# Kernel optimization log

Hardware: AMD Instinct MI355X
Metric: run time of the kernel (lower is better)

Reference implementation:

```python
import jax, jax.numpy as jnp
import numpy as np

N = 50000      # nodes
E = 800000     # edges
C = 128        # dim_feat / channels
D = 256        # dim_dense
OUT = 2        # dim_out
L = 5          # num_layers - 1 GCN2Conv layers
ALPHA = 0.1    # main_param -> GCN2Conv alpha; theta=None -> beta=1.0
SLOPE = 0.01   # LeakyReLU default negative slope


def setup_inputs() -> dict:
    key = jax.random.key(0)
    ks = jax.random.split(key, 6)
    x = jax.random.normal(ks[0], (N, C), jnp.float32)
    edge_index = jax.random.randint(ks[1], (2, E), 0, N, jnp.int32)
    conv_weights = jax.random.normal(ks[2], (L, C, C), jnp.float32) * (1.0 / np.sqrt(C))
    w_dense = jax.random.normal(ks[3], (C, D), jnp.float32) * (1.0 / np.sqrt(C))
    b_dense = jnp.zeros((D,), jnp.float32)
    w_out = jax.random.normal(ks[4], (D, OUT), jnp.float32) * (1.0 / np.sqrt(D))
    b_out = jnp.zeros((OUT,), jnp.float32)
    return dict(x=x, edge_index=edge_index, conv_weights=conv_weights,
                w_dense=w_dense, b_dense=b_dense, w_out=w_out, b_out=b_out)


def _gcn_norm(edge_index, num_nodes):
    """Symmetric gcn_norm with self-loops: returns row, col, D^-1/2 * D^-1/2 edge weights."""
    loop = jnp.arange(num_nodes, dtype=edge_index.dtype)
    row = jnp.concatenate([edge_index[0], loop])  # sources
    col = jnp.concatenate([edge_index[1], loop])  # targets (aggregation index)
    ones = jnp.ones(row.shape[0], jnp.float32)
    deg = jax.ops.segment_sum(ones, col, num_segments=num_nodes)
    dinv = jnp.where(deg > 0, jax.lax.rsqrt(jnp.maximum(deg, 1e-12)), 0.0)
    return row, col, dinv[row] * dinv[col]


def reference(x, edge_index, conv_weights, w_dense, b_dense, w_out, b_out):
    num_nodes = x.shape[0]
    row, col, norm = _gcn_norm(edge_index, num_nodes)
    x0 = x
    for l in range(conv_weights.shape[0]):
        # propagate: h[i] = sum_{j->i} norm * x[j]   (gather -> scatter-add)
        h = jax.ops.segment_sum(norm[:, None] * x[row], col, num_segments=num_nodes)
        # GCN2Conv with shared_weights=True, beta=1 (theta=None): out = ((1-a)h + a*x0) @ W
        out = (1.0 - ALPHA) * h + ALPHA * x0
        x = jax.nn.leaky_relu(out @ conv_weights[l], negative_slope=SLOPE)
    x = x @ w_dense + b_dense
    return x @ w_out + b_out
```

## Files before the change

kernel.cpp:

```cpp
#include <hip/hip_runtime.h>
#include <hip/hip_fp16.h>

#define C 128
#define NOUT 2
#define ALPHA 0.1f
#define SLOPE 0.01f
#define ZP 136

typedef _Float16 half4v __attribute__((ext_vector_type(4)));
typedef float float4v __attribute__((ext_vector_type(4)));


__global__ __launch_bounds__(256) void count_prep_kernel(
    const int* __restrict__ col, int* __restrict__ cnt, int* __restrict__ rank, int E,
    const float* __restrict__ x, __half* __restrict__ xh, int n,
    const float* __restrict__ W, _Float16* __restrict__ WT, int wtot,
    const float* __restrict__ wd, _Float16* __restrict__ WDT,
    int CB, int CV, int WTB)
{
    int b = blockIdx.x;
    if (b < CB) {
        int base = b * 1024 + threadIdx.x;
        #pragma unroll
        for (int j = 0; j < 4; ++j) {
            int e = base + j * 256;
            if (e < E) rank[e] = atomicAdd(&cnt[col[e]], 1);
        }
    } else if (b < CB + CV) {
        int g = (b - CB) * 256 + threadIdx.x;
        if (g >= n * 32) return;
        float4 v = ((const float4*)x)[g];
        union { __half2 h; unsigned u; } a2, b2;
        a2.h = __float22half2_rn(make_float2(v.x, v.y));
        b2.h = __float22half2_rn(make_float2(v.z, v.w));
        ((uint2*)xh)[g] = make_uint2(a2.u, b2.u);
    } else if (b < CB + CV + WTB) {
        int idx = (b - CB - CV) * 256 + threadIdx.x;
        if (idx >= wtot) return;
        int l = idx >> 14, rem = idx & 16383;
        int nrow = rem >> 7, kk = rem & 127;
        WT[idx] = (_Float16)W[(l << 14) + kk * C + nrow];
    } else {
        int idx = (b - CB - CV - WTB) * 256 + threadIdx.x;
        if (idx >= 256 * C) return;
        int nrow = idx >> 7, kk = idx & 127;
        WDT[idx] = (_Float16)wd[kk * 256 + nrow];
    }
}

__global__ __launch_bounds__(1024) void scanA_kernel(const int* __restrict__ cnt,
                                                     int* __restrict__ offs,
                                                     int* __restrict__ bsum,
                                                     float* __restrict__ dinv, int n) {
    __shared__ int wsum[16];
    int t = threadIdx.x, lane = t & 63, wv = t >> 6;
    int i = blockIdx.x * 1024 + t;
    int v = (i < n) ? cnt[i] : 0;
    if (i < n) dinv[i] = rsqrtf((float)(v + 1));
    int sc = v;
    #pragma unroll
    for (int d = 1; d < 64; d <<= 1) {
        int u = __shfl_up(sc, d);
        if (lane >= d) sc += u;
    }
    if (lane == 63) wsum[wv] = sc;
    __syncthreads();
    int woff = 0;
    #pragma unroll
    for (int j = 0; j < 16; ++j) woff += (j < wv) ? wsum[j] : 0;
    if (i < n) offs[i] = woff + sc - v;
    if (t == 0) {
        int tot = 0;
        #pragma unroll
        for (int j = 0; j < 16; ++j) tot += wsum[j];
        bsum[blockIdx.x] = tot;
    }
}

__global__ __launch_bounds__(1024) void scanB_kernel(const int* __restrict__ bsum,
                                                     int* __restrict__ bbase, int nb) {
    __shared__ int wsum[16];
    int t = threadIdx.x, lane = t & 63, wv = t >> 6;
    int v = (t < nb) ? bsum[t] : 0;
    int sc = v;
    #pragma unroll
    for (int d = 1; d < 64; d <<= 1) {
        int u = __shfl_up(sc, d);
        if (lane >= d) sc += u;
    }
    if (lane == 63) wsum[wv] = sc;
    __syncthreads();
    int woff = 0;
    #pragma unroll
    for (int j = 0; j < 16; ++j) woff += (j < wv) ? wsum[j] : 0;
    if (t < nb) bbase[t] = woff + sc - v;
}

__global__ void scanC_kernel(int* __restrict__ offs, const int* __restrict__ bbase,
                             int n, int E) {
    int i = blockIdx.x * 256 + threadIdx.x;
    if (i < n) offs[i] = offs[i] + bbase[i >> 10];
    if (i == n) offs[n] = E;
}

__global__ void fill_kernel(const int* __restrict__ row, const int* __restrict__ col,
                            const float* __restrict__ dinv, const int* __restrict__ offs,
                            const int* __restrict__ rank, unsigned* __restrict__ csr, int E) {
    int base = blockIdx.x * 2048 + threadIdx.x;
    #pragma unroll
    for (int j = 0; j < 8; ++j) {
        int e = base + j * 256;
        if (e < E) {
            int r = row[e], c = col[e];
            union { __half h; unsigned short u; } nh;
            nh.h = __float2half_rn(dinv[r] * dinv[c]);
            csr[offs[c] + rank[e]] = ((unsigned)r << 16) | (unsigned)nh.u;
        }
    }
}

__device__ __forceinline__ void accum8(float* a, uint4 q, float w) {
    union { unsigned u; __half2 h; } c;
    float2 f;
    c.u = q.x; f = __half22float2(c.h); a[0] += w * f.x; a[1] += w * f.y;
    c.u = q.y; f = __half22float2(c.h); a[2] += w * f.x; a[3] += w * f.y;
    c.u = q.z; f = __half22float2(c.h); a[4] += w * f.x; a[5] += w * f.y;
    c.u = q.w; f = __half22float2(c.h); a[6] += w * f.x; a[7] += w * f.y;
}

__device__ __forceinline__ uint4 pack8(const float* a) {
    union { __half2 h; unsigned u; } c0, c1, c2, c3;
    c0.h = __float22half2_rn(make_float2(a[0], a[1]));
    c1.h = __float22half2_rn(make_float2(a[2], a[3]));
    c2.h = __float22half2_rn(make_float2(a[4], a[5]));
    c3.h = __float22half2_rn(make_float2(a[6], a[7]));
    return make_uint4(c0.u, c1.u, c2.u, c3.u);
}

__device__ __forceinline__ float norm_of(unsigned m) {
    union { unsigned short u; __half h; } nh;
    nh.u = (unsigned short)(m & 0xffffu);
    return __half2float(nh.h);
}

__global__ __launch_bounds__(256) void agg_kernel(
    const __half* __restrict__ xc, const __half* __restrict__ x0h,
    const int* __restrict__ offs, const unsigned* __restrict__ csr,
    const float* __restrict__ dinv, __half* __restrict__ z, int n)
{
    int node = blockIdx.x * 8 + (threadIdx.x >> 5);
    if (node >= n) return;
    int l32 = threadIdx.x & 31;
    int sub = l32 >> 4;
    int cg = l32 & 15;
    const uint4* x4 = (const uint4*)xc;
    uint4 qs = x4[(size_t)node * 16 + cg];
    uint4 q0x = ((const uint4*)x0h)[(size_t)node * 16 + cg];
    float di = dinv[node];

    float a0[8] = {}, a1[8] = {}, a2[8] = {}, a3[8] = {};
    int beg = offs[node], end = offs[node + 1];
    int k = beg + sub;
    for (; k + 14 < end; k += 16) {
        unsigned m0 = csr[k], m1 = csr[k + 2], m2 = csr[k + 4], m3 = csr[k + 6];
        unsigned m4 = csr[k + 8], m5 = csr[k + 10], m6 = csr[k + 12], m7 = csr[k + 14];
        uint4 q0 = x4[(size_t)(m0 >> 16) * 16 + cg];
        uint4 q1 = x4[(size_t)(m1 >> 16) * 16 + cg];
        uint4 q2 = x4[(size_t)(m2 >> 16) * 16 + cg];
        uint4 q3 = x4[(size_t)(m3 >> 16) * 16 + cg];
        uint4 q4 = x4[(size_t)(m4 >> 16) * 16 + cg];
        uint4 q5 = x4[(size_t)(m5 >> 16) * 16 + cg];
        uint4 q6 = x4[(size_t)(m6 >> 16) * 16 + cg];
        uint4 q7 = x4[(size_t)(m7 >> 16) * 16 + cg];
        accum8(a0, q0, norm_of(m0));
        accum8(a1, q1, norm_of(m1));
        accum8(a2, q2, norm_of(m2));
        accum8(a3, q3, norm_of(m3));
        accum8(a0, q4, norm_of(m4));
        accum8(a1, q5, norm_of(m5));
        accum8(a2, q6, norm_of(m6));
        accum8(a3, q7, norm_of(m7));
    }
    for (; k + 6 < end; k += 8) {
        unsigned m0 = csr[k], m1 = csr[k + 2], m2 = csr[k + 4], m3 = csr[k + 6];
        uint4 q0 = x4[(size_t)(m0 >> 16) * 16 + cg];
        uint4 q1 = x4[(size_t)(m1 >> 16) * 16 + cg];
        uint4 q2 = x4[(size_t)(m2 >> 16) * 16 + cg];
        uint4 q3 = x4[(size_t)(m3 >> 16) * 16 + cg];
        accum8(a0, q0, norm_of(m0));
        accum8(a1, q1, norm_of(m1));
        accum8(a2, q2, norm_of(m2));
        accum8(a3, q3, norm_of(m3));
    }
    for (; k < end; k += 2) {
        unsigned m = csr[k];
        uint4 q = x4[(size_t)(m >> 16) * 16 + cg];
        accum8(a0, q, norm_of(m));
    }
    #pragma unroll
    for (int j = 0; j < 8; ++j) a0[j] += a1[j] + a2[j] + a3[j];
    #pragma unroll
    for (int j = 0; j < 8; ++j) a0[j] += __shfl_xor(a0[j], 16);
    if (sub == 0) {
        float sw = di * di;
        accum8(a0, qs, sw);
        float xr[8] = {};
        accum8(xr, q0x, 1.f);
        float zz[8];
        #pragma unroll
        for (int j = 0; j < 8; ++j) zz[j] = (1.f - ALPHA) * a0[j] + ALPHA * xr[j];
        ((uint4*)z)[(size_t)node * 16 + cg] = pack8(zz);
    }
}

__global__ __launch_bounds__(256) void layer_mfma(
    const __half* __restrict__ zin, const _Float16* __restrict__ WT,
    __half* __restrict__ xn, int n)
{
    __shared__ _Float16 zl[64 * ZP];
    int i0 = blockIdx.x * 64;
    int t = threadIdx.x;
    int w = t >> 6, lane = t & 63;
    int c = lane & 15, g = lane >> 4;

    const uint4* z4 = (const uint4*)zin;
    #pragma unroll
    for (int p = t; p < 64 * 16; p += 256) {
        int r = p >> 4, c8 = p & 15;
        uint4 zv = make_uint4(0, 0, 0, 0);
        if (i0 + r < n) zv = z4[(size_t)(i0 + r) * 16 + c8];
        *(uint4*)&zl[r * ZP + c8 * 8] = zv;
    }

    half4v bf[8][2];
    #pragma unroll
    for (int kb = 0; kb < 8; ++kb)
        #pragma unroll
        for (int nt = 0; nt < 2; ++nt)
            bf[kb][nt] = *(const half4v*)&WT[((w * 2 + nt) * 16 + c) * C + kb * 16 + 4 * g];

    __syncthreads();

    #pragma unroll
    for (int m = 0; m < 4; ++m) {
        const _Float16* arow = &zl[(m * 16 + c) * ZP];
        half4v af[8];
        #pragma unroll
        for (int kb = 0; kb < 8; ++kb) af[kb] = *(const half4v*)&arow[kb * 16 + 4 * g];
        float4v acc0 = (float4v)0.f, acc1 = (float4v)0.f;
        #pragma unroll
        for (int kb = 0; kb < 8; ++kb) {
            acc0 = __builtin_amdgcn_mfma_f32_16x16x16f16(af[kb], bf[kb][0], acc0, 0, 0, 0);
            acc1 = __builtin_amdgcn_mfma_f32_16x16x16f16(af[kb], bf[kb][1], acc1, 0, 0, 0);
        }
        #pragma unroll
        for (int r = 0; r < 4; ++r) {
            int node = i0 + m * 16 + 4 * g + r;
            if (node < n) {
                float v0 = acc0[r]; v0 = v0 > 0.f ? v0 : SLOPE * v0;
                float v1 = acc1[r]; v1 = v1 > 0.f ? v1 : SLOPE * v1;
                xn[(size_t)node * C + w * 32 + c]      = __float2half_rn(v0);
                xn[(size_t)node * C + w * 32 + 16 + c] = __float2half_rn(v1);
            }
        }
    }
}

__global__ __launch_bounds__(256) void dense_mfma(
    const __half* __restrict__ xin, const _Float16* __restrict__ WDT,
    const float* __restrict__ bd, const float* __restrict__ wo,
    const float* __restrict__ bo, float* __restrict__ out, int n)
{
    __shared__ _Float16 xl[64 * ZP];
    __shared__ float pp[64][4][2];
    int i0 = blockIdx.x * 64;
    int t = threadIdx.x;
    int w = t >> 6, lane = t & 63;
    int c = lane & 15, g = lane >> 4;

    const uint4* g4 = (const uint4*)xin;
    for (int p = t; p < 64 * 16; p += 256) {
        int r = p >> 4, c8 = p & 15;
        uint4 v = make_uint4(0, 0, 0, 0);
        if (i0 + r < n) v = g4[(size_t)(i0 + r) * 16 + c8];
        *(uint4*)&xl[r * ZP + c8 * 8] = v;
    }

    half4v bf[8][4];
    #pragma unroll
    for (int kb = 0; kb < 8; ++kb)
        #pragma unroll
        for (int nt = 0; nt < 4; ++nt)
            bf[kb][nt] = *(const half4v*)&WDT[((w * 4 + nt) * 16 + c) * C + kb * 16 + 4 * g];
    float bdv[4], wo0[4], wo1[4];
    #pragma unroll
    for (int nt = 0; nt < 4; ++nt) {
        int coln = (w * 4 + nt) * 16 + c;
        bdv[nt] = bd[coln];
        wo0[nt] = wo[coln * 2 + 0];
        wo1[nt] = wo[coln * 2 + 1];
    }

    __syncthreads();

    #pragma unroll
    for (int m = 0; m < 4; ++m) {
        const _Float16* arow = &xl[(m * 16 + c) * ZP];
        half4v af[8];
        #pragma unroll
        for (int kb = 0; kb < 8; ++kb) af[kb] = *(const half4v*)&arow[kb * 16 + 4 * g];
        float4v acc[4];
        #pragma unroll
        for (int nt = 0; nt < 4; ++nt) acc[nt] = (float4v)0.f;
        #pragma unroll
        for (int kb = 0; kb < 8; ++kb) {
            #pragma unroll
            for (int nt = 0; nt < 4; ++nt)
                acc[nt] = __builtin_amdgcn_mfma_f32_16x16x16f16(af[kb], bf[kb][nt], acc[nt], 0, 0, 0);
        }
        float p0[4] = {0.f, 0.f, 0.f, 0.f}, p1[4] = {0.f, 0.f, 0.f, 0.f};
        #pragma unroll
        for (int nt = 0; nt < 4; ++nt) {
            #pragma unroll
            for (int r = 0; r < 4; ++r) {
                float hv = acc[nt][r] + bdv[nt];
                p0[r] += hv * wo0[nt];
                p1[r] += hv * wo1[nt];
            }
        }
        #pragma unroll
        for (int ms = 1; ms <= 8; ms <<= 1) {
            #pragma unroll
            for (int r = 0; r < 4; ++r) {
                p0[r] += __shfl_xor(p0[r], ms);
                p1[r] += __shfl_xor(p1[r], ms);
            }
        }
        if (c == 0) {
            #pragma unroll
            for (int r = 0; r < 4; ++r) {
                pp[m * 16 + 4 * g + r][w][0] = p0[r];
                pp[m * 16 + 4 * g + r][w][1] = p1[r];
            }
        }
    }
    __syncthreads();
    if (t < 128) {
        int r = t >> 1, o = t & 1;
        int node = i0 + r;
        if (node < n) {
            float s = pp[r][0][o] + pp[r][1][o] + pp[r][2][o] + pp[r][3][o];
            out[(size_t)node * NOUT + o] = s + bo[o];
        }
    }
}

extern "C" void kernel_launch(void* const* d_in, const int* in_sizes, int n_in,
                              void* d_out, int out_size, void* d_ws, size_t ws_size,
                              hipStream_t stream) {
    const float* x0    = (const float*)d_in[0];
    const int*   ei    = (const int*)d_in[1];
    const float* convW = (const float*)d_in[2];
    const float* wd    = (const float*)d_in[3];
    const float* bd    = (const float*)d_in[4];
    const float* wo    = (const float*)d_in[5];
    const float* bo    = (const float*)d_in[6];
    float* out = (float*)d_out;

    int N = in_sizes[0] / C;
    int E = in_sizes[1] / 2;
    int L = in_sizes[2] / (C * C);
    const int* row = ei;
    const int* col = ei + E;
    int NB = (N + 1023) / 1024;

    char* p = (char*)d_ws;
    auto alloc = [&](size_t bytes) {
        char* r = p;
        p += (bytes + 255) & ~(size_t)255;
        return r;
    };
    int*      cnt    = (int*)alloc((size_t)N * 4);
    int*      offs   = (int*)alloc((size_t)(N + 1) * 4);
    int*      rank   = (int*)alloc((size_t)E * 4);
    int*      bsum   = (int*)alloc((size_t)NB * 4);
    int*      bbase  = (int*)alloc((size_t)NB * 4);
    unsigned* csr    = (unsigned*)alloc((size_t)E * 4);
    float*    dinv   = (float*)alloc((size_t)N * 4);
    __half*   x0h    = (__half*)alloc((size_t)N * C * 2);
    __half*   bufA   = (__half*)alloc((size_t)N * C * 2);
    __half*   zbuf   = (__half*)alloc((size_t)N * C * 2);
    _Float16* WT     = (_Float16*)alloc((size_t)L * C * C * 2);
    _Float16* WDT    = (_Float16*)alloc((size_t)256 * C * 2);

    int wtot = L * C * C;
    int CB  = (E + 1023) / 1024;
    int CV  = (N * 32 + 255) / 256;
    int WTB = (wtot + 255) / 256;
    int WDB = (256 * C + 255) / 256;

    hipMemsetAsync(cnt, 0, (size_t)N * 4, stream);
    count_prep_kernel<<<CB + CV + WTB + WDB, 256, 0, stream>>>(
        col, cnt, rank, E, x0, x0h, N, convW, WT, wtot, wd, WDT, CB, CV, WTB);
    scanA_kernel<<<NB, 1024, 0, stream>>>(cnt, offs, bsum, dinv, N);
    scanB_kernel<<<1, 1024, 0, stream>>>(bsum, bbase, NB);
    scanC_kernel<<<(N + 256) / 256, 256, 0, stream>>>(offs, bbase, N, E);
    fill_kernel<<<(E + 2047) / 2048, 256, 0, stream>>>(row, col, dinv, offs, rank, csr, E);

    const __half* xc = x0h;
    for (int l = 0; l < L; ++l) {
        agg_kernel<<<(N + 7) / 8, 256, 0, stream>>>(xc, x0h, offs, csr, dinv, zbuf, N);
        layer_mfma<<<(N + 63) / 64, 256, 0, stream>>>(zbuf, WT + (size_t)l * C * C,
                                                      bufA, N);
        xc = bufA;
    }
    dense_mfma<<<(N + 63) / 64, 256, 0, stream>>>(xc, WDT, bd, wo, bo, out, N);
}
```

Baseline: 368.5 us.

## Split node features into channel-chunk planes and aggregate each chunk separately

Feature buffers move from row-major [N][128] to 8 planes of [N][16] half, and the aggregation grid runs one block per (node group, chunk). The idea is that each gathered chunk plane (about 1.6 MB) fits in cache better, so random neighbour gathers hit L2 more often. In exchange every edge index is read eight times, the per-lane gather shrinks to 32 bytes, and loads and stores in the MFMA kernels are remapped to the new layout. The count kernel is also retuned to process 2048 edges per block.

New measurement: 609.0 us. 65.3% more time.

```diff
diff --git a/kernel.cpp b/kernel.cpp
--- a/kernel.cpp
+++ b/kernel.cpp
@@ -6,6 +6,7 @@
 #define ALPHA 0.1f
 #define SLOPE 0.01f
 #define ZP 136
+#define NCH 8
 
 typedef _Float16 half4v __attribute__((ext_vector_type(4)));
 typedef float float4v __attribute__((ext_vector_type(4)));
@@ -20,20 +21,23 @@
 {
     int b = blockIdx.x;
     if (b < CB) {
-        int base = b * 1024 + threadIdx.x;
-        #pragma unroll
-        for (int j = 0; j < 4; ++j) {
+        int base = b * 2048 + threadIdx.x;
+        #pragma unroll
+        for (int j = 0; j < 8; ++j) {
             int e = base + j * 256;
             if (e < E) rank[e] = atomicAdd(&cnt[col[e]], 1);
         }
     } else if (b < CB + CV) {
         int g = (b - CB) * 256 + threadIdx.x;
         if (g >= n * 32) return;
+        int node = g >> 5, c4q = g & 31;
         float4 v = ((const float4*)x)[g];
         union { __half2 h; unsigned u; } a2, b2;
         a2.h = __float22half2_rn(make_float2(v.x, v.y));
         b2.h = __float22half2_rn(make_float2(v.z, v.w));
-        ((uint2*)xh)[g] = make_uint2(a2.u, b2.u);
+        int chunk = c4q >> 2, pos = c4q & 3;
+        ((uint2*)xh)[(size_t)chunk * (n * 4) + (size_t)node * 4 + pos] =
+            make_uint2(a2.u, b2.u);
     } else if (b < CB + CV + WTB) {
         int idx = (b - CB - CV) * 256 + threadIdx.x;
         if (idx >= wtot) return;
@@ -148,60 +152,43 @@
     const int* __restrict__ offs, const unsigned* __restrict__ csr,
     const float* __restrict__ dinv, __half* __restrict__ z, int n)
 {
-    int node = blockIdx.x * 8 + (threadIdx.x >> 5);
+    int wg = blockIdx.x;
+    int chunk = wg & 7;
+    int node = (wg >> 3) * 8 + (threadIdx.x >> 5);
     if (node >= n) return;
     int l32 = threadIdx.x & 31;
-    int sub = l32 >> 4;
-    int cg = l32 & 15;
-    const uint4* x4 = (const uint4*)xc;
-    uint4 qs = x4[(size_t)node * 16 + cg];
-    uint4 q0x = ((const uint4*)x0h)[(size_t)node * 16 + cg];
+    int slot = l32 >> 1;
+    int chl = l32 & 1;
+    const uint4* x4 = (const uint4*)xc + (size_t)chunk * n * 2;
+    const uint4* x04 = (const uint4*)x0h + (size_t)chunk * n * 2;
+    uint4 qs = x4[(size_t)node * 2 + chl];
+    uint4 q0x = x04[(size_t)node * 2 + chl];
     float di = dinv[node];
 
-    float a0[8] = {}, a1[8] = {}, a2[8] = {}, a3[8] = {};
+    float a0[8] = {}, a1[8] = {};
     int beg = offs[node], end = offs[node + 1];
-    int k = beg + sub;
-    for (; k + 14 < end; k += 16) {
-        unsigned m0 = csr[k], m1 = csr[k + 2], m2 = csr[k + 4], m3 = csr[k + 6];
-        unsigned m4 = csr[k + 8], m5 = csr[k + 10], m6 = csr[k + 12], m7 = csr[k + 14];
-        uint4 q0 = x4[(size_t)(m0 >> 16) * 16 + cg];
-        uint4 q1 = x4[(size_t)(m1 >> 16) * 16 + cg];
-        uint4 q2 = x4[(size_t)(m2 >> 16) * 16 + cg];
-        uint4 q3 = x4[(size_t)(m3 >> 16) * 16 + cg];
-        uint4 q4 = x4[(size_t)(m4 >> 16) * 16 + cg];
-        uint4 q5 = x4[(size_t)(m5 >> 16) * 16 + cg];
-        uint4 q6 = x4[(size_t)(m6 >> 16) * 16 + cg];
-        uint4 q7 = x4[(size_t)(m7 >> 16) * 16 + cg];
+    int k = beg + slot;
+    for (; k + 16 < end; k += 32) {
+        unsigned m0 = __builtin_nontemporal_load(&csr[k]);
+        unsigned m1 = __builtin_nontemporal_load(&csr[k + 16]);
+        uint4 q0 = x4[(size_t)(m0 >> 16) * 2 + chl];
+        uint4 q1 = x4[(size_t)(m1 >> 16) * 2 + chl];
         accum8(a0, q0, norm_of(m0));
         accum8(a1, q1, norm_of(m1));
-        accum8(a2, q2, norm_of(m2));
-        accum8(a3, q3, norm_of(m3));
-        accum8(a0, q4, norm_of(m4));
-        accum8(a1, q5, norm_of(m5));
-        accum8(a2, q6, norm_of(m6));
-        accum8(a3, q7, norm_of(m7));
-    }
-    for (; k + 6 < end; k += 8) {
-        unsigned m0 = csr[k], m1 = csr[k + 2], m2 = csr[k + 4], m3 = csr[k + 6];
-        uint4 q0 = x4[(size_t)(m0 >> 16) * 16 + cg];
-        uint4 q1 = x4[(size_t)(m1 >> 16) * 16 + cg];
-        uint4 q2 = x4[(size_t)(m2 >> 16) * 16 + cg];
-        uint4 q3 = x4[(size_t)(m3 >> 16) * 16 + cg];
-        accum8(a0, q0, norm_of(m0));
-        accum8(a1, q1, norm_of(m1));
-        accum8(a2, q2, norm_of(m2));
-        accum8(a3, q3, norm_of(m3));
-    }
-    for (; k < end; k += 2) {
-        unsigned m = csr[k];
-        uint4 q = x4[(size_t)(m >> 16) * 16 + cg];
+    }
+    if (k < end) {
+        unsigned m = __builtin_nontemporal_load(&csr[k]);
+        uint4 q = x4[(size_t)(m >> 16) * 2 + chl];
         accum8(a0, q, norm_of(m));
     }
     #pragma unroll
-    for (int j = 0; j < 8; ++j) a0[j] += a1[j] + a2[j] + a3[j];
-    #pragma unroll
-    for (int j = 0; j < 8; ++j) a0[j] += __shfl_xor(a0[j], 16);
-    if (sub == 0) {
+    for (int j = 0; j < 8; ++j) a0[j] += a1[j];
+    #pragma unroll
+    for (int ms = 2; ms <= 16; ms <<= 1) {
+        #pragma unroll
+        for (int j = 0; j < 8; ++j) a0[j] += __shfl_xor(a0[j], ms);
+    }
+    if (slot == 0) {
         float sw = di * di;
         accum8(a0, qs, sw);
         float xr[8] = {};
@@ -209,7 +196,7 @@
         float zz[8];
         #pragma unroll
         for (int j = 0; j < 8; ++j) zz[j] = (1.f - ALPHA) * a0[j] + ALPHA * xr[j];
-        ((uint4*)z)[(size_t)node * 16 + cg] = pack8(zz);
+        ((uint4*)z)[(size_t)chunk * n * 2 + (size_t)node * 2 + chl] = pack8(zz);
     }
 }
 
@@ -225,11 +212,14 @@
 
     const uint4* z4 = (const uint4*)zin;
     #pragma unroll
-    for (int p = t; p < 64 * 16; p += 256) {
-        int r = p >> 4, c8 = p & 15;
+    for (int q = 0; q < 4; ++q) {
+        int idx = q * 256 + t;
+        int chunk = idx >> 7;
+        int within = idx & 127;
+        int r = within >> 1, u = within & 1;
         uint4 zv = make_uint4(0, 0, 0, 0);
-        if (i0 + r < n) zv = z4[(size_t)(i0 + r) * 16 + c8];
-        *(uint4*)&zl[r * ZP + c8 * 8] = zv;
+        if (i0 + r < n) zv = z4[(size_t)chunk * n * 2 + (size_t)(i0 + r) * 2 + u];
+        *(uint4*)&zl[r * ZP + chunk * 16 + u * 8] = zv;
     }
 
     half4v bf[8][2];
@@ -259,8 +249,8 @@
             if (node < n) {
                 float v0 = acc0[r]; v0 = v0 > 0.f ? v0 : SLOPE * v0;
                 float v1 = acc1[r]; v1 = v1 > 0.f ? v1 : SLOPE * v1;
-                xn[(size_t)node * C + w * 32 + c]      = __float2half_rn(v0);
-                xn[(size_t)node * C + w * 32 + 16 + c] = __float2half_rn(v1);
+                xn[(size_t)(2 * w) * (n * 16) + (size_t)node * 16 + c] = __float2half_rn(v0);
+                xn[(size_t)(2 * w + 1) * (n * 16) + (size_t)node * 16 + c] = __float2half_rn(v1);
             }
         }
     }
@@ -279,11 +269,15 @@
     int c = lane & 15, g = lane >> 4;
 
     const uint4* g4 = (const uint4*)xin;
-    for (int p = t; p < 64 * 16; p += 256) {
-        int r = p >> 4, c8 = p & 15;
+    #pragma unroll
+    for (int q = 0; q < 4; ++q) {
+        int idx = q * 256 + t;
+        int chunk = idx >> 7;
+        int within = idx & 127;
+        int r = within >> 1, u = within & 1;
         uint4 v = make_uint4(0, 0, 0, 0);
-        if (i0 + r < n) v = g4[(size_t)(i0 + r) * 16 + c8];
-        *(uint4*)&xl[r * ZP + c8 * 8] = v;
+        if (i0 + r < n) v = g4[(size_t)chunk * n * 2 + (size_t)(i0 + r) * 2 + u];
+        *(uint4*)&xl[r * ZP + chunk * 16 + u * 8] = v;
     }
 
     half4v bf[8][4];
@@ -394,7 +388,7 @@
     _Float16* WDT    = (_Float16*)alloc((size_t)256 * C * 2);
 
     int wtot = L * C * C;
-    int CB  = (E + 1023) / 1024;
+    int CB  = (E + 2047) / 2048;
     int CV  = (N * 32 + 255) / 256;
     int WTB = (wtot + 255) / 256;
     int WDB = (256 * C + 255) / 256;
@@ -408,8 +402,9 @@
     fill_kernel<<<(E + 2047) / 2048, 256, 0, stream>>>(row, col, dinv, offs, rank, csr, E);
 
     const __half* xc = x0h;
+    int aggGrid = ((N + 7) / 8) * NCH;
     for (int l = 0; l < L; ++l) {
-        agg_kernel<<<(N + 7) / 8, 256, 0, stream>>>(xc, x0h, offs, csr, dinv, zbuf, N);
+        agg_kernel<<<aggGrid, 256, 0, stream>>>(xc, x0h, offs, csr, dinv, zbuf, N);
         layer_mfma<<<(N + 63) / 64, 256, 0, stream>>>(zbuf, WT + (size_t)l * C * C,
                                                       bufA, N);
         xc = bufA;
```
